# Kernel tuning notes

Hardware: AMD Instinct MI355X
Metric: run time of the kernel (lower is better)

Reference implementation:

```python
import jax, jax.numpy as jnp
import numpy as np

Z_DIM = 3
H = 128
N_BLOCKS = 4
N = 30000
E = 180000
T = 2


def _mlp2(x, W1, b1, W2, b2):
    return jnp.maximum(x @ W1 + b1, 0.0) @ W2 + b2


def _stats(x, eps=1e-8):
    # batch mean/std as accumulated by the running-stat Normalizer (buffers -> no grad)
    m = x.mean(0)
    v = jnp.maximum((x * x).mean(0) - m * m, 0.0)
    s = jnp.maximum(jnp.sqrt(v), eps)
    return jax.lax.stop_gradient(m), jax.lax.stop_gradient(s)


def setup_inputs() -> dict:
    key = jax.random.key(0)
    ks = jax.random.split(key, 32)

    def w(k, shape, fan_in):
        return jax.random.normal(k, shape, jnp.float32) / np.sqrt(fan_in).astype(np.float32)

    inp = {}
    inp["z"] = jax.random.normal(ks[0], (T, N, Z_DIM), jnp.float32)
    inp["z_target"] = jax.random.normal(ks[1], (N, Z_DIM), jnp.float32)
    inp["pos"] = jax.random.uniform(ks[2], (N, 2), jnp.float32)
    # encoder node MLP: z_dim -> H -> H
    inp["enc_node_W1"] = w(ks[3], (Z_DIM, H), Z_DIM)
    inp["enc_node_b1"] = jnp.zeros((H,), jnp.float32)
    inp["enc_node_W2"] = w(ks[4], (H, H), H)
    inp["enc_node_b2"] = jnp.zeros((H,), jnp.float32)
    # encoder edge MLP: edge_dim(3) -> H -> H
    inp["enc_edge_W1"] = w(ks[5], (3, H), 3)
    inp["enc_edge_b1"] = jnp.zeros((H,), jnp.float32)
    inp["enc_edge_W2"] = w(ks[6], (H, H), H)
    inp["enc_edge_b2"] = jnp.zeros((H,), jnp.float32)
    # decoder MLP: H -> H -> z_dim
    inp["dec_W1"] = w(ks[7], (H, H), H)
    inp["dec_b1"] = jnp.zeros((H,), jnp.float32)
    inp["dec_W2"] = w(ks[8], (H, Z_DIM), H)
    inp["dec_b2"] = jnp.zeros((Z_DIM,), jnp.float32)
    # GraphNetBlocks, stacked over n_blocks
    inp["blk_edge_W1"] = w(ks[9], (N_BLOCKS, 3 * H, H), 3 * H)
    inp["blk_edge_b1"] = jnp.zeros((N_BLOCKS, H), jnp.float32)
    inp["blk_edge_W2"] = w(ks[10], (N_BLOCKS, H, H), H)
    inp["blk_edge_b2"] = jnp.zeros((N_BLOCKS, H), jnp.float32)
    inp["blk_node_W1"] = w(ks[11], (N_BLOCKS, 2 * H, H), 2 * H)
    inp["blk_node_b1"] = jnp.zeros((N_BLOCKS, H), jnp.float32)
    inp["blk_node_W2"] = w(ks[12], (N_BLOCKS, H, H), H)
    inp["blk_node_b2"] = jnp.zeros((N_BLOCKS, H), jnp.float32)
    # bidirectional mesh edges (triangles_to_edges output)
    inp["senders"] = jax.random.randint(ks[13], (E,), 0, N, jnp.int64)
    inp["receivers"] = jax.random.randint(ks[14], (E,), 0, N, jnp.int64)
    return inp


def reference(z, z_target, pos,
              enc_node_W1, enc_node_b1, enc_node_W2, enc_node_b2,
              enc_edge_W1, enc_edge_b1, enc_edge_W2, enc_edge_b2,
              dec_W1, dec_b1, dec_W2, dec_b2,
              blk_edge_W1, blk_edge_b1, blk_edge_W2, blk_edge_b2,
              blk_node_W1, blk_node_b1, blk_node_W2, blk_node_b2,
              senders, receivers):
    zl = z[-1]                                   # [N, z_dim]
    n_nodes = zl.shape[0]

    # --- build_graph ---
    rel = pos[senders] - pos[receivers]          # [E, 2]
    ef_raw = jnp.concatenate([rel, jnp.linalg.norm(rel, axis=1, keepdims=True)], axis=1)  # [E, 3]
    em, es = _stats(ef_raw)
    ef = _mlp2((ef_raw - em) / es, enc_edge_W1, enc_edge_b1, enc_edge_W2, enc_edge_b2)    # [E, H]
    nm, ns = _stats(zl)
    nf = _mlp2((zl - nm) / ns, enc_node_W1, enc_node_b1, enc_node_W2, enc_node_b2)        # [N, H]

    # --- message passing blocks ---
    def block(carry, p):
        nf, ef = carry
        eW1, eb1, eW2, eb2, nW1, nb1, nW2, nb2 = p
        e_in = jnp.concatenate([ef, nf[senders], nf[receivers]], axis=1)   # [E, 3H]
        ef = _mlp2(e_in, eW1, eb1, eW2, eb2) + ef
        agg = jax.ops.segment_sum(ef, receivers, num_segments=n_nodes)    # [N, H]
        n_in = jnp.concatenate([nf, agg], axis=1)                          # [N, 2H]
        nf = _mlp2(n_in, nW1, nb1, nW2, nb2) + nf
        return (nf, ef), None

    (nf, ef), _ = jax.lax.scan(block, (nf, ef),
                               (blk_edge_W1, blk_edge_b1, blk_edge_W2, blk_edge_b2,
                                blk_node_W1, blk_node_b1, blk_node_W2, blk_node_b2))

    # --- decode + loss ---
    output = _mlp2(nf, dec_W1, dec_b1, dec_W2, dec_b2)                     # [N, z_dim]
    target = z_target - zl
    om, os = _stats(target)
    target_normalized = (target - om) / os
    loss = jnp.mean((target_normalized - output) ** 2)

    z_update = jax.lax.stop_gradient(output) * os + om                     # Normalizer.inverse(detach)
    z_pred = zl + z_update
    rmse = jnp.mean(jnp.sqrt(jnp.mean((z_pred - z_target) ** 2, axis=0)))
    return z_pred, loss, rmse
```

## Files before the change

### kernel.cpp

```cpp
#include <hip/hip_runtime.h>
#include <hip/hip_bf16.h>
#include <math.h>

#define HDIM 128
#define TPB 256

typedef __attribute__((ext_vector_type(8))) short bf16x8;
typedef __attribute__((ext_vector_type(4))) float f32x4;

static inline int ceil_div(int a, int b){ return (a + b - 1) / b; }

__device__ __forceinline__ float wave_sum(float v){
#pragma unroll
  for (int o = 32; o > 0; o >>= 1) v += __shfl_down(v, o, 64);
  return v;
}
__device__ __forceinline__ int wave_sum_i(int v){
#pragma unroll
  for (int o = 32; o > 0; o >>= 1) v += __shfl_down(v, o, 64);
  return v;
}

__device__ __forceinline__ short f2bf(float f){
  __hip_bfloat16 h = __float2bfloat16(f);
  return *reinterpret_cast<short*>(&h);
}
__device__ __forceinline__ float bfb2f(short s){
  unsigned int u = ((unsigned int)(unsigned short)s) << 16;
  return __builtin_bit_cast(float, u);
}

__device__ __forceinline__ void gl_lds16(const short* g, short* l){
  __builtin_amdgcn_global_load_lds(
      (const __attribute__((address_space(1))) void*)g,
      (__attribute__((address_space(3))) void*)l, 16, 0, 0);
}

__global__ void prep_a(const int* __restrict__ rcv, int* __restrict__ deg, int E, int neb,
                       const float* __restrict__ zl, const float* __restrict__ zt,
                       float* __restrict__ npart, int N, int nnb,
                       const float* __restrict__ encEW2,
                       const float* __restrict__ encNW2,
                       const float* __restrict__ decW1,
                       const float* __restrict__ beW1,
                       const float* __restrict__ beW2,
                       const float* __restrict__ bnW1,
                       const float* __restrict__ bnW2,
                       __hip_bfloat16* __restrict__ wp){
  __shared__ float red[4][12];
  const int bx = blockIdx.x, tid = threadIdx.x;
  if (bx < neb){
    int e = bx * 256 + tid;
    if (e < E) atomicAdd(&deg[rcv[e]], 1);
    return;
  }
  if (bx < neb + nnb){
    int b = bx - neb;
    int w = tid >> 6, l = tid & 63;
    int n = b * 256 + tid;
    float s[12];
#pragma unroll
    for (int i = 0; i < 12; i++) s[i] = 0.f;
    if (n < N){
#pragma unroll
      for (int d = 0; d < 3; d++){
        float z = zl[3*n+d];
        float t = zt[3*n+d] - z;
        s[d]   = z;  s[3+d] = z*z;
        s[6+d] = t;  s[9+d] = t*t;
      }
    }
#pragma unroll
    for (int i = 0; i < 12; i++) s[i] = wave_sum(s[i]);
    if (l == 0)
#pragma unroll
      for (int i = 0; i < 12; i++) red[w][i] = s[i];
    __syncthreads();
    if (tid < 12)
      npart[(size_t)b * 12 + tid] =
        red[0][tid] + red[1][tid] + red[2][tid] + red[3][tid];
    return;
  }
  int pid = bx - neb - nnb;
  int y = pid / 192;
  int x = pid - y * 192;
  const float* src; __hip_bfloat16* dst; int K;
  if (y == 0){ src = encEW2; dst = wp;          K = 128; }
  else if (y == 1){ src = encNW2; dst = wp + 16384; K = 128; }
  else if (y == 2){ src = decW1;  dst = wp + 32768; K = 128; }
  else {
    int b = (y - 3) >> 2, j = (y - 3) & 3;
    __hip_bfloat16* base = wp + 49152 + b * 114688;
    if (j == 0){ src = beW1 + b*49152; dst = base;          K = 384; }
    else if (j == 1){ src = beW2 + b*16384; dst = base + 49152; K = 128; }
    else if (j == 2){ src = bnW1 + b*32768; dst = base + 65536; K = 256; }
    else { src = bnW2 + b*16384; dst = base + 98304; K = 128; }
  }
  int id = x * 256 + tid;
  if (id >= 128 * K) return;
  int c = id >> 12;
  int r = id & 4095;
  int t = r >> 9;
  int l = (r >> 3) & 63;
  int j = r & 7;
  int k = c * 32 + ((l >> 4) << 3) + j;
  int n = t * 16 + (l & 15);
  dst[id] = __float2bfloat16(src[k * 128 + n]);
}

__global__ void scan_pass1(const int* __restrict__ deg, int* __restrict__ bsum, int N){
  __shared__ int red[4];
  int tid = threadIdx.x;
  int base = blockIdx.x * 1024;
  int s = 0;
  for (int i = tid; i < 1024; i += 256){
    int idx = base + i;
    if (idx < N) s += deg[idx];
  }
  s = wave_sum_i(s);
  if ((tid & 63) == 0) red[tid >> 6] = s;
  __syncthreads();
  if (tid == 0) bsum[blockIdx.x] = red[0] + red[1] + red[2] + red[3];
}

__global__ void scan_pass3(const int* __restrict__ deg, const int* __restrict__ bsum,
                           int nsb, int* __restrict__ cursor, int N){
  __shared__ int tsum[256];
  __shared__ int base_s;
  int tid = threadIdx.x;
  if (tid == 0){
    int acc = 0;
    for (int b = 0; b < (int)blockIdx.x; b++) acc += bsum[b];
    base_s = acc;
  }
  int base = blockIdx.x * 1024;
  int i0 = base + tid * 4;
  int v[4];
  int s = 0;
#pragma unroll
  for (int k = 0; k < 4; k++){
    int idx = i0 + k;
    v[k] = (idx < N) ? deg[idx] : 0;
    s += v[k];
  }
  tsum[tid] = s;
  __syncthreads();
  for (int off = 1; off < 256; off <<= 1){
    int val = (tid >= off) ? tsum[tid - off] : 0;
    __syncthreads();
    tsum[tid] += val;
    __syncthreads();
  }
  int excl = (tid == 0) ? 0 : tsum[tid - 1];
  int b = base_s + excl;
#pragma unroll
  for (int k = 0; k < 4; k++){
    int idx = i0 + k;
    if (idx < N){
      cursor[idx] = b;
      b += v[k];
    }
  }
}

__global__ void edge_prep(const float* __restrict__ pos,
                          const int* __restrict__ snd,
                          const int* __restrict__ rcv,
                          int* __restrict__ cursor,
                          int* __restrict__ psnd,
                          int* __restrict__ prcv,
                          float* __restrict__ ef_raw,
                          float* __restrict__ epart, int E){
  __shared__ float red[4][6];
  int tid = threadIdx.x, w = tid >> 6, l = tid & 63;
  int e = blockIdx.x * blockDim.x + tid;
  float s[6] = {0.f,0.f,0.f,0.f,0.f,0.f};
  if (e < E){
    int si = snd[e], ri = rcv[e];
    int p = atomicAdd(&cursor[ri], 1);
    psnd[p] = si;
    prcv[p] = ri;
    float rx = pos[2*si]   - pos[2*ri];
    float ry = pos[2*si+1] - pos[2*ri+1];
    float nm = sqrtf(rx*rx + ry*ry);
    ef_raw[3*p]   = rx;
    ef_raw[3*p+1] = ry;
    ef_raw[3*p+2] = nm;
    s[0] = rx; s[1] = ry; s[2] = nm;
    s[3] = rx*rx; s[4] = ry*ry; s[5] = nm*nm;
  }
#pragma unroll
  for (int k = 0; k < 6; k++) s[k] = wave_sum(s[k]);
  if (l == 0)
#pragma unroll
    for (int k = 0; k < 6; k++) red[w][k] = s[k];
  __syncthreads();
  if (tid < 6)
    epart[(size_t)blockIdx.x * 6 + tid] =
      red[0][tid] + red[1][tid] + red[2][tid] + red[3][tid];
}

__global__ void reduce_finalize(const float* __restrict__ ep, int ne,
                                const float* __restrict__ np_, int nn,
                                float* __restrict__ fin, int E, int N){
  __shared__ float red[4];
  __shared__ float raw[18];
  int tid = threadIdx.x, w = tid >> 6, l = tid & 63;
  for (int j = 0; j < 6; j++){
    float s = 0.f;
    for (int b = tid; b < ne; b += 256) s += ep[(size_t)b * 6 + j];
    s = wave_sum(s);
    if (l == 0) red[w] = s;
    __syncthreads();
    if (tid == 0) raw[j] = red[0] + red[1] + red[2] + red[3];
    __syncthreads();
  }
  for (int j = 0; j < 12; j++){
    float s = 0.f;
    for (int b = tid; b < nn; b += 256) s += np_[(size_t)b * 12 + j];
    s = wave_sum(s);
    if (l == 0) red[w] = s;
    __syncthreads();
    if (tid == 0) raw[6 + j] = red[0] + red[1] + red[2] + red[3];
    __syncthreads();
  }
  if (tid == 0){
#pragma unroll
    for (int d = 0; d < 3; d++){
      float cE = (float)E, cN = (float)N;
      float m, v;
      m = raw[0+d] / cE; v = fmaxf(raw[3+d]/cE - m*m, 0.f);
      fin[0+d] = m;  fin[3+d]  = fmaxf(sqrtf(v), 1e-8f);
      m = raw[6+d] / cN; v = fmaxf(raw[9+d]/cN - m*m, 0.f);
      fin[6+d] = m;  fin[9+d]  = fmaxf(sqrtf(v), 1e-8f);
      m = raw[12+d] / cN; v = fmaxf(raw[15+d]/cN - m*m, 0.f);
      fin[12+d] = m; fin[15+d] = fmaxf(sqrtf(v), 1e-8f);
    }
  }
}

__launch_bounds__(256)
__global__ void encoder_both(const float* __restrict__ eraw,
                             const float* __restrict__ zl,
                             const float* __restrict__ fin,
                             const float* __restrict__ eW1, const float* __restrict__ eb1,
                             const float* __restrict__ nW1, const float* __restrict__ nb1,
                             const __hip_bfloat16* __restrict__ wp,
                             const float* __restrict__ eb2, const float* __restrict__ nb2,
                             __hip_bfloat16* __restrict__ efo, __hip_bfloat16* __restrict__ nfo,
                             int E, int N, int EB){
  __shared__ __align__(16) short bsh[16384];
  const int tid = threadIdx.x, w = tid >> 6, l = tid & 63, m = l & 15, q = l >> 4;
  const bool ise = ((int)blockIdx.x < EB);
  const float* raw = ise ? eraw : zl;
  const float* mptr = fin + (ise ? 0 : 6);
  const float* sptr = fin + (ise ? 3 : 9);
  const float* W1 = ise ? eW1 : nW1;
  const float* b1 = ise ? eb1 : nb1;
  const float* b2 = ise ? eb2 : nb2;
  const short* wsrc = (const short*)wp + (ise ? 0 : 16384);
  __hip_bfloat16* out = ise ? efo : nfo;
  const int rows = ise ? E : N;
  const int bx = ise ? (int)blockIdx.x : (int)blockIdx.x - EB;
#pragma unroll
  for (int i = 0; i < 8; i++){
    int inst = w * 8 + i;
    gl_lds16(wsrc + inst * 512 + l * 8, &bsh[inst * 512]);
  }
  float s0 = mptr[0], s1 = mptr[1], s2 = mptr[2];
  float d0 = sptr[0], d1 = sptr[1], d2 = sptr[2];
  const int row0 = bx * 64 + w * 16;
  const int ra = min(row0 + m, rows - 1);
  float x0 = (raw[3*ra]   - s0) / d0;
  float x1 = (raw[3*ra+1] - s1) / d1;
  float x2 = (raw[3*ra+2] - s2) / d2;
  bf16x8 afr[4];
#pragma unroll
  for (int c = 0; c < 4; c++){
    int nb = c * 32 + q * 8;
#pragma unroll
    for (int j = 0; j < 8; j++){
      float h = b1[nb+j] + x0 * W1[nb+j] + x1 * W1[128+nb+j] + x2 * W1[256+nb+j];
      afr[c][j] = f2bf(fmaxf(h, 0.f));
    }
  }
  f32x4 acc[8];
#pragma unroll
  for (int t = 0; t < 8; t++) acc[t] = (f32x4){0.f,0.f,0.f,0.f};
  __syncthreads();
#pragma unroll
  for (int c = 0; c < 4; c++){
#pragma unroll
    for (int t = 0; t < 8; t++){
      bf16x8 b = *(const bf16x8*)&bsh[(c*8 + t)*512 + l*8];
      acc[t] = __builtin_amdgcn_mfma_f32_16x16x32_bf16(afr[c], b, acc[t], 0, 0, 0);
    }
  }
  const int row_d = row0 + q * 4;
#pragma unroll
  for (int t = 0; t < 8; t++){
    int col = t * 16 + m;
    float bb = b2[col];
#pragma unroll
    for (int r = 0; r < 4; r++){
      int e = row_d + r;
      if (e < rows) out[(size_t)e * HDIM + col] = __float2bfloat16(acc[t][r] + bb);
    }
  }
}

__launch_bounds__(256)
__global__ void msg_pre(const __hip_bfloat16* __restrict__ nf,
                        const __hip_bfloat16* __restrict__ eWf,
                        __hip_bfloat16* __restrict__ u,
                        float* __restrict__ agg, int N){
  __shared__ __align__(16) short wsh[16384];
  const int tid = threadIdx.x, w = tid >> 6, l = tid & 63, m = l & 15, q = l >> 4;
  const short* wsrc = (const short*)eWf + 4 * 4096;
#pragma unroll
  for (int i = 0; i < 8; i++){
    int f = w * 8 + i;
    gl_lds16(wsrc + f * 512 + l * 8, &wsh[f * 512]);
  }
  {
    float* az = agg + (size_t)blockIdx.x * 8192;
#pragma unroll
    for (int i = 0; i < 8; i++)
      *(f32x4*)(az + (size_t)(i * 256 + tid) * 4) = (f32x4){0.f,0.f,0.f,0.f};
  }
  const int row0 = blockIdx.x * 64 + w * 16;
  const int ra = min(row0 + m, N - 1);
  const short* pa = (const short*)nf + (size_t)ra * HDIM + q * 8;
  bf16x8 afr[4];
#pragma unroll
  for (int c = 0; c < 4; c++) afr[c] = *(const bf16x8*)(pa + c * 32);
  f32x4 acc[8];
#pragma unroll
  for (int t = 0; t < 8; t++) acc[t] = (f32x4){0.f,0.f,0.f,0.f};
  __syncthreads();
#pragma unroll
  for (int c = 0; c < 4; c++)
#pragma unroll
    for (int t = 0; t < 8; t++){
      bf16x8 b = *(const bf16x8*)&wsh[(c*8 + t)*512 + l*8];
      acc[t] = __builtin_amdgcn_mfma_f32_16x16x32_bf16(afr[c], b, acc[t], 0, 0, 0);
    }
  const int row_d = row0 + q * 4;
#pragma unroll
  for (int t = 0; t < 8; t++){
    int col = t * 16 + m;
#pragma unroll
    for (int r = 0; r < 4; r++){
      int n = row_d + r;
      if (n < N) u[(size_t)n * 256 + col] = __float2bfloat16(acc[t][r]);
    }
  }
  __syncthreads();
#pragma unroll
  for (int i = 0; i < 8; i++){
    int f = w * 8 + i;
    gl_lds16(wsrc + 16384 + f * 512 + l * 8, &wsh[f * 512]);
  }
#pragma unroll
  for (int t = 0; t < 8; t++) acc[t] = (f32x4){0.f,0.f,0.f,0.f};
  __syncthreads();
#pragma unroll
  for (int c = 0; c < 4; c++)
#pragma unroll
    for (int t = 0; t < 8; t++){
      bf16x8 b = *(const bf16x8*)&wsh[(c*8 + t)*512 + l*8];
      acc[t] = __builtin_amdgcn_mfma_f32_16x16x32_bf16(afr[c], b, acc[t], 0, 0, 0);
    }
#pragma unroll
  for (int t = 0; t < 8; t++){
    int col = 128 + t * 16 + m;
#pragma unroll
    for (int r = 0; r < 4; r++){
      int n = row_d + r;
      if (n < N) u[(size_t)n * 256 + col] = __float2bfloat16(acc[t][r]);
    }
  }
}

__launch_bounds__(512)
__global__ void edge_block(const int* __restrict__ psnd,
                           const int* __restrict__ prcv,
                           const __hip_bfloat16* __restrict__ u,
                           __hip_bfloat16* __restrict__ ef,
                           const __hip_bfloat16* __restrict__ Wfrag,
                           const float* __restrict__ b1,
                           const float* __restrict__ b2,
                           float* __restrict__ agg,
                           int do_write, int E){
  __shared__ __align__(16) short bsh[16384];
  __shared__ __align__(16) short hsh[8][16][136];
  __shared__ int rsh[128];
  const int tid = threadIdx.x, w = tid >> 6, l = tid & 63, m = l & 15, q = l >> 4;
  const short* wsrc = (const short*)Wfrag;
  const int row0 = blockIdx.x * 128 + w * 16;
  const int grow = min(row0 + (l >> 2), E - 1);
  const int us_row = psnd[grow], ur_row = prcv[grow];
  if ((l & 3) == 0) rsh[w * 16 + (l >> 2)] = ur_row;
#pragma unroll
  for (int i = 0; i < 4; i++){
    int inst = i * 8 + w;
    gl_lds16(wsrc + inst * 512 + l * 8, &bsh[inst * 512]);
  }
  const int ra = min(row0 + m, E - 1);
  const short* pe = (const short*)ef + (size_t)ra * HDIM + q * 8;
  bf16x8 afr[4];
#pragma unroll
  for (int c = 0; c < 4; c++) afr[c] = *(const bf16x8*)(pe + c * 32);
  {
    const short* pus = (const short*)u + (size_t)us_row * 256 + (l & 3) * 32;
    const short* pur = (const short*)u + (size_t)ur_row * 256 + 128 + (l & 3) * 32;
    short* hdst = &hsh[w][l >> 2][(l & 3) * 32];
#pragma unroll
    for (int k = 0; k < 4; k++){
      bf16x8 a = *(const bf16x8*)(pus + k * 8);
      bf16x8 b = *(const bf16x8*)(pur + k * 8);
      bf16x8 s;
#pragma unroll
      for (int j = 0; j < 8; j++) s[j] = f2bf(bfb2f(a[j]) + bfb2f(b[j]));
      *(bf16x8*)(hdst + k * 8) = s;
    }
  }
  f32x4 acc[8];
#pragma unroll
  for (int t = 0; t < 8; t++) acc[t] = (f32x4){0.f,0.f,0.f,0.f};
  __syncthreads();
#pragma unroll
  for (int c = 0; c < 4; c++){
#pragma unroll
    for (int t = 0; t < 8; t++){
      bf16x8 b = *(const bf16x8*)&bsh[(c*8 + t)*512 + l*8];
      acc[t] = __builtin_amdgcn_mfma_f32_16x16x32_bf16(afr[c], b, acc[t], 0, 0, 0);
    }
  }
  __syncthreads();
#pragma unroll
  for (int i = 0; i < 4; i++){
    int inst = i * 8 + w;
    gl_lds16(wsrc + 49152 + inst * 512 + l * 8, &bsh[inst * 512]);
  }
#pragma unroll
  for (int t = 0; t < 8; t++){
    float bb = b1[t * 16 + m];
#pragma unroll
    for (int r = 0; r < 4; r++){
      float uval = bfb2f(hsh[w][q*4 + r][t*16 + m]);
      hsh[w][q*4 + r][t*16 + m] = f2bf(fmaxf(acc[t][r] + uval + bb, 0.f));
    }
  }
  __syncthreads();
  bf16x8 ah[4];
  const short* ph = &hsh[w][m][0] + q * 8;
#pragma unroll
  for (int c = 0; c < 4; c++) ah[c] = *(const bf16x8*)(ph + c * 32);
#pragma unroll
  for (int t = 0; t < 8; t++) acc[t] = (f32x4){0.f,0.f,0.f,0.f};
#pragma unroll
  for (int c = 0; c < 4; c++){
#pragma unroll
    for (int t = 0; t < 8; t++){
      bf16x8 b = *(const bf16x8*)&bsh[(c*8 + t)*512 + l*8];
      acc[t] = __builtin_amdgcn_mfma_f32_16x16x32_bf16(ah[c], b, acc[t], 0, 0, 0);
    }
  }
#pragma unroll
  for (int t = 0; t < 8; t++){
    float bb = b2[t * 16 + m];
#pragma unroll
    for (int r = 0; r < 4; r++)
      hsh[w][q*4 + r][t*16 + m] = f2bf(acc[t][r] + bb);
  }
  const int orow = row0 + (l >> 2);
  const int orc = min(orow, E - 1);
  const short* pold = (const short*)ef + (size_t)orc * HDIM + (l & 3) * 32;
  short* hslot = &hsh[w][l >> 2][(l & 3) * 32];
  short* dst = (short*)ef + (size_t)orc * HDIM + (l & 3) * 32;
  const bool wr = (orow < E) && do_write;
#pragma unroll
  for (int k = 0; k < 4; k++){
    bf16x8 vnew = *(const bf16x8*)(hslot + k * 8);
    bf16x8 vo   = *(const bf16x8*)(pold + k * 8);
    bf16x8 vr;
#pragma unroll
    for (int j = 0; j < 8; j++) vr[j] = f2bf(bfb2f(vnew[j]) + bfb2f(vo[j]));
    *(bf16x8*)(hslot + k * 8) = vr;
    if (wr) *(bf16x8*)(dst + k * 8) = vr;
  }
  __syncthreads();
  {
    const int c = tid & 127;
    const int g = tid >> 7;
    const int nval = min(128, E - (int)blockIdx.x * 128);
    const int e0 = g * 32;
    if (e0 < nval){
      const int e1 = min(e0 + 32, nval);
      float run = 0.f; int cur = -1; int runstart = e0;
#pragma unroll
      for (int half = 0; half < 2; half++){
        float v[16]; int rv[16];
#pragma unroll
        for (int k = 0; k < 16; k++){
          int e = e0 + half * 16 + k;
          v[k]  = bfb2f(hsh[(e >> 4) & 7][e & 15][c]);
          rv[k] = rsh[e & 127];
        }
#pragma unroll
        for (int k = 0; k < 16; k++){
          int e = e0 + half * 16 + k;
          if (e < e1){
            if (rv[k] != cur){
              if (cur >= 0){
                if (runstart == e0) atomicAdd(&agg[(size_t)cur * 128 + c], run);
                else                agg[(size_t)cur * 128 + c] = run;
              }
              cur = rv[k]; run = 0.f; runstart = e;
            }
            run += v[k];
          }
        }
      }
      atomicAdd(&agg[(size_t)cur * 128 + c], run);
    }
  }
}

#define NB_COMPUTE_CHUNK(c) do {                                               \
  const short* bb_ = &bsh[(((c) >> 1) & 1) * 8192 + ((c) & 1) * 4096];         \
  _Pragma("unroll")                                                            \
  for (int t = 0; t < 8; t++){                                                 \
    bf16x8 b = *(const bf16x8*)(bb_ + t * 512 + l * 8);                        \
    acc[t] = __builtin_amdgcn_mfma_f32_16x16x32_bf16(afr[c], b, acc[t], 0, 0, 0); \
  }                                                                            \
} while(0)

__launch_bounds__(256)
__global__ void node_block(const float* __restrict__ agg,
                           __hip_bfloat16* __restrict__ nf,
                           const __hip_bfloat16* __restrict__ Wfrag,
                           const float* __restrict__ b1,
                           const float* __restrict__ b2,
                           int N){
  __shared__ __align__(16) short bsh[16384];
  __shared__ __align__(16) short hsh[4][16][136];
  const int tid = threadIdx.x, w = tid >> 6, l = tid & 63, m = l & 15, q = l >> 4;
  const short* wsrc = (const short*)Wfrag;
  auto stage_pair = [&](int p){
    const short* s = wsrc + p * 8192;
    short* d = &bsh[(p & 1) * 8192];
#pragma unroll
    for (int i = 0; i < 4; i++)
      gl_lds16(s + (i*4 + w)*512 + l*8, d + (i*4 + w)*512);
  };
  stage_pair(0); stage_pair(1);

  const int row0 = blockIdx.x * 64 + w * 16;
  const int ra = min(row0 + m, N - 1);
  const short* pn = (const short*)nf + (size_t)ra * HDIM + q * 8;
  bf16x8 afr[8];
#pragma unroll
  for (int c = 0; c < 4; c++) afr[c] = *(const bf16x8*)(pn + c * 32);

  const float* pag = agg + (size_t)ra * 128 + q * 8;
#pragma unroll
  for (int c = 0; c < 4; c++){
    f32x4 a0 = *(const f32x4*)(pag + c * 32);
    f32x4 a1 = *(const f32x4*)(pag + c * 32 + 4);
#pragma unroll
    for (int j = 0; j < 4; j++){
      afr[4 + c][j]     = f2bf(a0[j]);
      afr[4 + c][4 + j] = f2bf(a1[j]);
    }
  }

  f32x4 acc[8];
#pragma unroll
  for (int t = 0; t < 8; t++) acc[t] = (f32x4){0.f,0.f,0.f,0.f};
  __syncthreads();
  NB_COMPUTE_CHUNK(0);
  NB_COMPUTE_CHUNK(1);
  __syncthreads();
  stage_pair(2);
  NB_COMPUTE_CHUNK(2);
  NB_COMPUTE_CHUNK(3);
  __syncthreads();
  stage_pair(3);
  NB_COMPUTE_CHUNK(4);
  NB_COMPUTE_CHUNK(5);
  __syncthreads();
  NB_COMPUTE_CHUNK(6);
  NB_COMPUTE_CHUNK(7);
  __syncthreads();
  {
    const short* s = wsrc + 32768;
#pragma unroll
    for (int i = 0; i < 8; i++)
      gl_lds16(s + (i*4 + w)*512 + l*8, &bsh[(i*4 + w)*512]);
  }
#pragma unroll
  for (int t = 0; t < 8; t++){
    float bb = b1[t * 16 + m];
#pragma unroll
    for (int r = 0; r < 4; r++)
      hsh[w][q*4 + r][t*16 + m] = f2bf(fmaxf(acc[t][r] + bb, 0.f));
  }
  __syncthreads();
  const short* ph = &hsh[w][m][0] + q * 8;
#pragma unroll
  for (int t = 0; t < 8; t++) acc[t] = (f32x4){0.f,0.f,0.f,0.f};
#pragma unroll
  for (int c = 0; c < 4; c++){
    bf16x8 a = *(const bf16x8*)(ph + c * 32);
#pragma unroll
    for (int t = 0; t < 8; t++){
      bf16x8 b = *(const bf16x8*)&bsh[(c*8 + t)*512 + l*8];
      acc[t] = __builtin_amdgcn_mfma_f32_16x16x32_bf16(a, b, acc[t], 0, 0, 0);
    }
  }
#pragma unroll
  for (int t = 0; t < 8; t++){
    float bb = b2[t * 16 + m];
#pragma unroll
    for (int r = 0; r < 4; r++)
      hsh[w][q*4 + r][t*16 + m] = f2bf(acc[t][r] + bb);
  }
  const int orow = row0 + (l >> 2);
  if (orow < N){
    const short* pold = (const short*)nf + (size_t)orow * HDIM + (l & 3) * 32;
    const short* src = &hsh[w][l >> 2][(l & 3) * 32];
    short* dst = (short*)nf + (size_t)orow * HDIM + (l & 3) * 32;
#pragma unroll
    for (int k = 0; k < 4; k++){
      bf16x8 vnew = *(const bf16x8*)(src + k * 8);
      bf16x8 vo   = *(const bf16x8*)(pold + k * 8);
      bf16x8 vr;
#pragma unroll
      for (int j = 0; j < 8; j++) vr[j] = f2bf(bfb2f(vnew[j]) + bfb2f(vo[j]));
      *(bf16x8*)(dst + k * 8) = vr;
    }
  }
}

__launch_bounds__(256)
__global__ void dec_fused(const __hip_bfloat16* __restrict__ A,
                          const __hip_bfloat16* __restrict__ Wf,
                          const float* __restrict__ b1,
                          const float* __restrict__ W2,
                          const float* __restrict__ b2,
                          const float* __restrict__ zl,
                          const float* __restrict__ z_target,
                          const float* __restrict__ fin,
                          float* __restrict__ d_out,
                          float* __restrict__ lred,
                          unsigned int* __restrict__ cnt,
                          int N){
  __shared__ __align__(16) short bsh[16384];
  __shared__ float Wl[HDIM * 3];
  __shared__ float red[4][4];
  const int tid = threadIdx.x, w = tid >> 6, l = tid & 63, m = l & 15, q = l >> 4;
  const short* wsrc = (const short*)Wf;
#pragma unroll
  for (int i = 0; i < 8; i++){
    int inst = w * 8 + i;
    gl_lds16(wsrc + inst * 512 + l * 8, &bsh[inst * 512]);
  }
  for (int i = tid; i < HDIM * 3; i += 256) Wl[i] = W2[i];
  const int row0 = blockIdx.x * 64 + w * 16;
  const int ra = min(row0 + m, N - 1);
  const short* pa = (const short*)A + (size_t)ra * HDIM + q * 8;
  bf16x8 afr[4];
#pragma unroll
  for (int c = 0; c < 4; c++) afr[c] = *(const bf16x8*)(pa + c * 32);
  f32x4 acc[8];
#pragma unroll
  for (int t = 0; t < 8; t++) acc[t] = (f32x4){0.f,0.f,0.f,0.f};
  __syncthreads();
#pragma unroll
  for (int c = 0; c < 4; c++){
#pragma unroll
    for (int t = 0; t < 8; t++){
      bf16x8 b = *(const bf16x8*)&bsh[(c*8 + t)*512 + l*8];
      acc[t] = __builtin_amdgcn_mfma_f32_16x16x32_bf16(afr[c], b, acc[t], 0, 0, 0);
    }
  }
  float p0[4] = {0,0,0,0}, p1[4] = {0,0,0,0}, p2[4] = {0,0,0,0};
#pragma unroll
  for (int t = 0; t < 8; t++){
    int col = t * 16 + m;
    float bb = b1[col];
    float w0 = Wl[col*3], w1 = Wl[col*3+1], w2 = Wl[col*3+2];
#pragma unroll
    for (int r = 0; r < 4; r++){
      float h = fmaxf(acc[t][r] + bb, 0.f);
      p0[r] += h * w0; p1[r] += h * w1; p2[r] += h * w2;
    }
  }
#pragma unroll
  for (int r = 0; r < 4; r++){
#pragma unroll
    for (int o = 1; o < 16; o <<= 1){
      p0[r] += __shfl_xor(p0[r], o, 64);
      p1[r] += __shfl_xor(p1[r], o, 64);
      p2[r] += __shfl_xor(p2[r], o, 64);
    }
  }
  float s[4] = {0.f,0.f,0.f,0.f};
  if (m == 0){
#pragma unroll
    for (int r = 0; r < 4; r++){
      int n = row0 + q * 4 + r;
      if (n < N){
        float pd[3] = {p0[r], p1[r], p2[r]};
#pragma unroll
        for (int d = 0; d < 3; d++){
          float o   = pd[d] + b2[d];
          float om = fin[12 + d], os = fin[15 + d];
          float zld = zl[3*n + d];
          float zt  = z_target[3*n + d];
          float tn  = ((zt - zld) - om) / os;
          float diff = tn - o;
          s[0] += diff * diff;
          float zp = zld + o * os + om;
          d_out[3*n + d] = zp;
          float e = zp - zt;
          s[1 + d] += e * e;
        }
      }
    }
  }
#pragma unroll
  for (int k = 0; k < 4; k++) s[k] = wave_sum(s[k]);
  if (l == 0)
#pragma unroll
    for (int k = 0; k < 4; k++) red[w][k] = s[k];
  __syncthreads();
  if (tid < 4)
    atomicAdd(&lred[tid], red[0][tid] + red[1][tid] + red[2][tid] + red[3][tid]);
  __syncthreads();
  if (tid == 0){
    __threadfence();
    unsigned int t = atomicAdd(cnt, 1u);
    if (t == gridDim.x - 1){
      float vals[4];
#pragma unroll
      for (int k = 0; k < 4; k++) vals[k] = atomicAdd(&lred[k], 0.f);
      float cN = (float)N;
      float loss = vals[0] / (3.f * cN);
      float rmse = (sqrtf(vals[1]/cN) + sqrtf(vals[2]/cN) + sqrtf(vals[3]/cN)) / 3.f;
      d_out[(size_t)3 * N]     = loss;
      d_out[(size_t)3 * N + 1] = rmse;
    }
  }
}

extern "C" void kernel_launch(void* const* d_in, const int* in_sizes, int n_in,
                              void* d_out, int out_size, void* d_ws, size_t ws_size,
                              hipStream_t stream){
  const float* z           = (const float*)d_in[0];
  const float* z_target    = (const float*)d_in[1];
  const float* pos         = (const float*)d_in[2];
  const float* enc_node_W1 = (const float*)d_in[3];
  const float* enc_node_b1 = (const float*)d_in[4];
  const float* enc_node_W2 = (const float*)d_in[5];
  const float* enc_node_b2 = (const float*)d_in[6];
  const float* enc_edge_W1 = (const float*)d_in[7];
  const float* enc_edge_b1 = (const float*)d_in[8];
  const float* enc_edge_W2 = (const float*)d_in[9];
  const float* enc_edge_b2 = (const float*)d_in[10];
  const float* dec_W1      = (const float*)d_in[11];
  const float* dec_b1      = (const float*)d_in[12];
  const float* dec_W2      = (const float*)d_in[13];
  const float* dec_b2      = (const float*)d_in[14];
  const float* blk_edge_W1 = (const float*)d_in[15];
  const float* blk_edge_b1 = (const float*)d_in[16];
  const float* blk_edge_W2 = (const float*)d_in[17];
  const float* blk_edge_b2 = (const float*)d_in[18];
  const float* blk_node_W1 = (const float*)d_in[19];
  const float* blk_node_b1 = (const float*)d_in[20];
  const float* blk_node_W2 = (const float*)d_in[21];
  const float* blk_node_b2 = (const float*)d_in[22];
  const int*   senders     = (const int*)d_in[23];
  const int*   receivers   = (const int*)d_in[24];

  const int N = in_sizes[1] / 3;
  const int E = in_sizes[23];
  const float* zl = z + (size_t)N * 3;

  const int neb = ceil_div(E, TPB);
  const int nnb = ceil_div(N, TPB);
  const int nsb = ceil_div(N, 1024);
  const int EB  = ceil_div(E, 64);
  const int NB  = ceil_div(N, 64);

  char* p = (char*)d_ws;
  auto carve = [&](size_t bytes) -> char* {
    char* r = p; p += (bytes + 255) & ~(size_t)255; return r;
  };
  float* stats_fin = (float*)carve(32 * 4);
  float* epart     = (float*)carve((size_t)neb * 6 * 4);
  float* npart     = (float*)carve((size_t)nnb * 12 * 4);
  float* ef_raw    = (float*)carve((size_t)E * 3 * 4);
  int*   deg       = (int*)carve((size_t)(N + 16) * 4);
  float* lred      = (float*)(deg + N);
  unsigned int* cnt = (unsigned int*)(deg + N + 4);
  int*   bsum      = (int*)carve((size_t)(nsb + 1) * 4);
  int*   cursor    = (int*)carve((size_t)N * 4);
  int*   psnd      = (int*)carve((size_t)E * 4);
  int*   prcv      = (int*)carve((size_t)E * 4);
  float* agg       = (float*)carve(((size_t)N + 64) * 128 * 4);
  __hip_bfloat16* wp = (__hip_bfloat16*)carve((size_t)507904 * 2);
  __hip_bfloat16* ef = (__hip_bfloat16*)carve((size_t)E * HDIM * 2);
  __hip_bfloat16* nf = (__hip_bfloat16*)carve((size_t)N * HDIM * 2);
  __hip_bfloat16* u  = (__hip_bfloat16*)carve((size_t)N * 256 * 2);

  float* out = (float*)d_out;

  hipMemsetAsync(deg, 0, (size_t)(N + 16) * 4, stream);

  prep_a<<<neb + nnb + 3648, TPB, 0, stream>>>(receivers, deg, E, neb,
                                               zl, z_target, npart, N, nnb,
                                               enc_edge_W2, enc_node_W2, dec_W1,
                                               blk_edge_W1, blk_edge_W2,
                                               blk_node_W1, blk_node_W2, wp);
  scan_pass1<<<nsb, TPB, 0, stream>>>(deg, bsum, N);
  scan_pass3<<<nsb, TPB, 0, stream>>>(deg, bsum, nsb, cursor, N);
  edge_prep<<<neb, TPB, 0, stream>>>(pos, senders, receivers, cursor,
                                     psnd, prcv, ef_raw, epart, E);
  reduce_finalize<<<1, TPB, 0, stream>>>(epart, neb, npart, nnb, stats_fin, E, N);

  encoder_both<<<EB + NB, TPB, 0, stream>>>(ef_raw, zl, stats_fin,
                                            enc_edge_W1, enc_edge_b1,
                                            enc_node_W1, enc_node_b1,
                                            wp, enc_edge_b2, enc_node_b2,
                                            ef, nf, E, N, EB);

  for (int b = 0; b < 4; b++){
    const __hip_bfloat16* eWf = wp + 49152 + (size_t)b * 114688;
    const __hip_bfloat16* nWf = eWf + 65536;
    const float* eb1 = blk_edge_b1 + (size_t)b * 128;
    const float* eb2 = blk_edge_b2 + (size_t)b * 128;
    const float* nb1 = blk_node_b1 + (size_t)b * 128;
    const float* nb2 = blk_node_b2 + (size_t)b * 128;

    msg_pre<<<NB, TPB, 0, stream>>>(nf, eWf, u, agg, N);
    edge_block<<<ceil_div(E, 128), 512, 0, stream>>>(psnd, prcv, u, ef,
                                                     eWf, eb1, eb2, agg,
                                                     (b < 3) ? 1 : 0, E);
    node_block<<<NB, TPB, 0, stream>>>(agg, nf, nWf, nb1, nb2, N);
  }

  dec_fused<<<NB, TPB, 0, stream>>>(nf, wp + 32768, dec_b1, dec_W2, dec_b2,
                                    zl, z_target, stats_fin,
                                    out, lred, cnt, N);
}
```

Before: 488.9 us.

## Fuse stats finalize, next-block msg_pre, and decoder into producer kernels

Folds the single-block reduce_finalize into edge_prep as a last-block-done reduction using an atomic counter. Fuses the next block's msg_pre (node projection into u and zeroing agg) into the tail of node_block, and the decoder into the final node_block via a mode flag. The aim is fewer kernel launches and one fewer reload of node features per block. The cost is more LDS and registers in node_block, plus a serial last-block tail in edge_prep.

```diff
diff --git a/kernel.cpp b/kernel.cpp
--- a/kernel.cpp
+++ b/kernel.cpp
@@ -170,8 +170,15 @@
                           int* __restrict__ psnd,
                           int* __restrict__ prcv,
                           float* __restrict__ ef_raw,
-                          float* __restrict__ epart, int E){
+                          float* __restrict__ epart,
+                          const float* __restrict__ npart, int nn,
+                          float* __restrict__ fin,
+                          unsigned int* __restrict__ ep_cnt,
+                          int E, int N){
   __shared__ float red[4][6];
+  __shared__ float rawS[18];
+  __shared__ float redS[4];
+  __shared__ int doneS;
   int tid = threadIdx.x, w = tid >> 6, l = tid & 63;
   int e = blockIdx.x * blockDim.x + tid;
   float s[6] = {0.f,0.f,0.f,0.f,0.f,0.f};
@@ -198,30 +205,31 @@
   if (tid < 6)
     epart[(size_t)blockIdx.x * 6 + tid] =
       red[0][tid] + red[1][tid] + red[2][tid] + red[3][tid];
-}
-
-__global__ void reduce_finalize(const float* __restrict__ ep, int ne,
-                                const float* __restrict__ np_, int nn,
-                                float* __restrict__ fin, int E, int N){
-  __shared__ float red[4];
-  __shared__ float raw[18];
-  int tid = threadIdx.x, w = tid >> 6, l = tid & 63;
+  __syncthreads();
+  if (tid == 0){
+    __threadfence();
+    unsigned int t = atomicAdd(ep_cnt, 1u);
+    doneS = (t == gridDim.x - 1);
+  }
+  __syncthreads();
+  if (!doneS) return;
+  const int ne = gridDim.x;
   for (int j = 0; j < 6; j++){
-    float s = 0.f;
-    for (int b = tid; b < ne; b += 256) s += ep[(size_t)b * 6 + j];
-    s = wave_sum(s);
-    if (l == 0) red[w] = s;
-    __syncthreads();
-    if (tid == 0) raw[j] = red[0] + red[1] + red[2] + red[3];
+    float t = 0.f;
+    for (int b = tid; b < ne; b += 256) t += epart[(size_t)b * 6 + j];
+    t = wave_sum(t);
+    if (l == 0) redS[w] = t;
+    __syncthreads();
+    if (tid == 0) rawS[j] = redS[0] + redS[1] + redS[2] + redS[3];
     __syncthreads();
   }
   for (int j = 0; j < 12; j++){
-    float s = 0.f;
-    for (int b = tid; b < nn; b += 256) s += np_[(size_t)b * 12 + j];
-    s = wave_sum(s);
-    if (l == 0) red[w] = s;
-    __syncthreads();
-    if (tid == 0) raw[6 + j] = red[0] + red[1] + red[2] + red[3];
+    float t = 0.f;
+    for (int b = tid; b < nn; b += 256) t += npart[(size_t)b * 12 + j];
+    t = wave_sum(t);
+    if (l == 0) redS[w] = t;
+    __syncthreads();
+    if (tid == 0) rawS[6 + j] = redS[0] + redS[1] + redS[2] + redS[3];
     __syncthreads();
   }
   if (tid == 0){
@@ -229,11 +237,11 @@
     for (int d = 0; d < 3; d++){
       float cE = (float)E, cN = (float)N;
       float m, v;
-      m = raw[0+d] / cE; v = fmaxf(raw[3+d]/cE - m*m, 0.f);
+      m = rawS[0+d] / cE; v = fmaxf(rawS[3+d]/cE - m*m, 0.f);
       fin[0+d] = m;  fin[3+d]  = fmaxf(sqrtf(v), 1e-8f);
-      m = raw[6+d] / cN; v = fmaxf(raw[9+d]/cN - m*m, 0.f);
+      m = rawS[6+d] / cN; v = fmaxf(rawS[9+d]/cN - m*m, 0.f);
       fin[6+d] = m;  fin[9+d]  = fmaxf(sqrtf(v), 1e-8f);
-      m = raw[12+d] / cN; v = fmaxf(raw[15+d]/cN - m*m, 0.f);
+      m = rawS[12+d] / cN; v = fmaxf(rawS[15+d]/cN - m*m, 0.f);
       fin[12+d] = m; fin[15+d] = fmaxf(sqrtf(v), 1e-8f);
     }
   }
@@ -543,9 +551,25 @@
                            const __hip_bfloat16* __restrict__ Wfrag,
                            const float* __restrict__ b1,
                            const float* __restrict__ b2,
+                           const __hip_bfloat16* __restrict__ eWf_next,
+                           __hip_bfloat16* __restrict__ u,
+                           float* __restrict__ aggz,
+                           int mode,
+                           const __hip_bfloat16* __restrict__ decWf,
+                           const float* __restrict__ db1,
+                           const float* __restrict__ dW2,
+                           const float* __restrict__ db2,
+                           const float* __restrict__ zl,
+                           const float* __restrict__ z_target,
+                           const float* __restrict__ fin,
+                           float* __restrict__ d_out,
+                           float* __restrict__ lred,
+                           unsigned int* __restrict__ cnt,
                            int N){
   __shared__ __align__(16) short bsh[16384];
   __shared__ __align__(16) short hsh[4][16][136];
+  __shared__ float Wl[HDIM * 3];
+  __shared__ float redS[4][4];
   const int tid = threadIdx.x, w = tid >> 6, l = tid & 63, m = l & 15, q = l >> 4;
   const short* wsrc = (const short*)Wfrag;
   auto stage_pair = [&](int p){
@@ -580,6 +604,12 @@
 #pragma unroll
   for (int t = 0; t < 8; t++) acc[t] = (f32x4){0.f,0.f,0.f,0.f};
   __syncthreads();
+  if (mode == 0){
+    float* az = aggz + (size_t)blockIdx.x * 8192;
+#pragma unroll
+    for (int i = 0; i < 8; i++)
+      *(f32x4*)(az + (size_t)(i * 256 + tid) * 4) = (f32x4){0.f,0.f,0.f,0.f};
+  }
   NB_COMPUTE_CHUNK(0);
   NB_COMPUTE_CHUNK(1);
   __syncthreads();
@@ -627,131 +657,170 @@
     for (int r = 0; r < 4; r++)
       hsh[w][q*4 + r][t*16 + m] = f2bf(acc[t][r] + bb);
   }
-  const int orow = row0 + (l >> 2);
-  if (orow < N){
-    const short* pold = (const short*)nf + (size_t)orow * HDIM + (l & 3) * 32;
-    const short* src = &hsh[w][l >> 2][(l & 3) * 32];
-    short* dst = (short*)nf + (size_t)orow * HDIM + (l & 3) * 32;
+  {
+    const int orow = row0 + (l >> 2);
+    const int orc = min(orow, N - 1);
+    const short* pold = (const short*)nf + (size_t)orc * HDIM + (l & 3) * 32;
+    short* hslot = &hsh[w][l >> 2][(l & 3) * 32];
+    short* dst = (short*)nf + (size_t)orc * HDIM + (l & 3) * 32;
+    const bool wr = (orow < N) && (mode == 0);
 #pragma unroll
     for (int k = 0; k < 4; k++){
-      bf16x8 vnew = *(const bf16x8*)(src + k * 8);
+      bf16x8 vnew = *(const bf16x8*)(hslot + k * 8);
       bf16x8 vo   = *(const bf16x8*)(pold + k * 8);
       bf16x8 vr;
 #pragma unroll
       for (int j = 0; j < 8; j++) vr[j] = f2bf(bfb2f(vnew[j]) + bfb2f(vo[j]));
-      *(bf16x8*)(dst + k * 8) = vr;
-    }
-  }
-}
-
-__launch_bounds__(256)
-__global__ void dec_fused(const __hip_bfloat16* __restrict__ A,
-                          const __hip_bfloat16* __restrict__ Wf,
-                          const float* __restrict__ b1,
-                          const float* __restrict__ W2,
-                          const float* __restrict__ b2,
-                          const float* __restrict__ zl,
-                          const float* __restrict__ z_target,
-                          const float* __restrict__ fin,
-                          float* __restrict__ d_out,
-                          float* __restrict__ lred,
-                          unsigned int* __restrict__ cnt,
-                          int N){
-  __shared__ __align__(16) short bsh[16384];
-  __shared__ float Wl[HDIM * 3];
-  __shared__ float red[4][4];
-  const int tid = threadIdx.x, w = tid >> 6, l = tid & 63, m = l & 15, q = l >> 4;
-  const short* wsrc = (const short*)Wf;
-#pragma unroll
-  for (int i = 0; i < 8; i++){
-    int inst = w * 8 + i;
-    gl_lds16(wsrc + inst * 512 + l * 8, &bsh[inst * 512]);
-  }
-  for (int i = tid; i < HDIM * 3; i += 256) Wl[i] = W2[i];
-  const int row0 = blockIdx.x * 64 + w * 16;
-  const int ra = min(row0 + m, N - 1);
-  const short* pa = (const short*)A + (size_t)ra * HDIM + q * 8;
-  bf16x8 afr[4];
-#pragma unroll
-  for (int c = 0; c < 4; c++) afr[c] = *(const bf16x8*)(pa + c * 32);
-  f32x4 acc[8];
-#pragma unroll
-  for (int t = 0; t < 8; t++) acc[t] = (f32x4){0.f,0.f,0.f,0.f};
-  __syncthreads();
-#pragma unroll
-  for (int c = 0; c < 4; c++){
+      *(bf16x8*)(hslot + k * 8) = vr;
+      if (wr) *(bf16x8*)(dst + k * 8) = vr;
+    }
+  }
+
+  if (mode == 0){
+    const short* ws = (const short*)eWf_next + 4 * 4096;
+#pragma unroll
+    for (int i = 0; i < 8; i++){
+      int f = w * 8 + i;
+      gl_lds16(ws + f * 512 + l * 8, &bsh[f * 512]);
+    }
+    __syncthreads();
+    bf16x8 a2[4];
+    const short* ph2 = &hsh[w][m][0] + q * 8;
+#pragma unroll
+    for (int c = 0; c < 4; c++) a2[c] = *(const bf16x8*)(ph2 + c * 32);
+#pragma unroll
+    for (int t = 0; t < 8; t++) acc[t] = (f32x4){0.f,0.f,0.f,0.f};
+#pragma unroll
+    for (int c = 0; c < 4; c++)
+#pragma unroll
+      for (int t = 0; t < 8; t++){
+        bf16x8 b = *(const bf16x8*)&bsh[(c*8 + t)*512 + l*8];
+        acc[t] = __builtin_amdgcn_mfma_f32_16x16x32_bf16(a2[c], b, acc[t], 0, 0, 0);
+      }
+    const int row_d = row0 + q * 4;
 #pragma unroll
     for (int t = 0; t < 8; t++){
-      bf16x8 b = *(const bf16x8*)&bsh[(c*8 + t)*512 + l*8];
-      acc[t] = __builtin_amdgcn_mfma_f32_16x16x32_bf16(afr[c], b, acc[t], 0, 0, 0);
-    }
-  }
-  float p0[4] = {0,0,0,0}, p1[4] = {0,0,0,0}, p2[4] = {0,0,0,0};
-#pragma unroll
-  for (int t = 0; t < 8; t++){
-    int col = t * 16 + m;
-    float bb = b1[col];
-    float w0 = Wl[col*3], w1 = Wl[col*3+1], w2 = Wl[col*3+2];
+      int col = t * 16 + m;
+#pragma unroll
+      for (int r = 0; r < 4; r++){
+        int n = row_d + r;
+        if (n < N) u[(size_t)n * 256 + col] = __float2bfloat16(acc[t][r]);
+      }
+    }
+    __syncthreads();
+#pragma unroll
+    for (int i = 0; i < 8; i++){
+      int f = w * 8 + i;
+      gl_lds16(ws + 16384 + f * 512 + l * 8, &bsh[f * 512]);
+    }
+#pragma unroll
+    for (int t = 0; t < 8; t++) acc[t] = (f32x4){0.f,0.f,0.f,0.f};
+    __syncthreads();
+#pragma unroll
+    for (int c = 0; c < 4; c++)
+#pragma unroll
+      for (int t = 0; t < 8; t++){
+        bf16x8 b = *(const bf16x8*)&bsh[(c*8 + t)*512 + l*8];
+        acc[t] = __builtin_amdgcn_mfma_f32_16x16x32_bf16(a2[c], b, acc[t], 0, 0, 0);
+      }
+#pragma unroll
+    for (int t = 0; t < 8; t++){
+      int col = 128 + t * 16 + m;
+#pragma unroll
+      for (int r = 0; r < 4; r++){
+        int n = row_d + r;
+        if (n < N) u[(size_t)n * 256 + col] = __float2bfloat16(acc[t][r]);
+      }
+    }
+  } else {
+    const short* ws = (const short*)decWf;
+#pragma unroll
+    for (int i = 0; i < 8; i++){
+      int f = w * 8 + i;
+      gl_lds16(ws + f * 512 + l * 8, &bsh[f * 512]);
+    }
+    for (int i = tid; i < HDIM * 3; i += 256) Wl[i] = dW2[i];
+    __syncthreads();
+    bf16x8 a2[4];
+    const short* ph2 = &hsh[w][m][0] + q * 8;
+#pragma unroll
+    for (int c = 0; c < 4; c++) a2[c] = *(const bf16x8*)(ph2 + c * 32);
+#pragma unroll
+    for (int t = 0; t < 8; t++) acc[t] = (f32x4){0.f,0.f,0.f,0.f};
+#pragma unroll
+    for (int c = 0; c < 4; c++)
+#pragma unroll
+      for (int t = 0; t < 8; t++){
+        bf16x8 b = *(const bf16x8*)&bsh[(c*8 + t)*512 + l*8];
+        acc[t] = __builtin_amdgcn_mfma_f32_16x16x32_bf16(a2[c], b, acc[t], 0, 0, 0);
+      }
+    float p0[4] = {0,0,0,0}, p1[4] = {0,0,0,0}, p2[4] = {0,0,0,0};
+#pragma unroll
+    for (int t = 0; t < 8; t++){
+      int col = t * 16 + m;
+      float bb = db1[col];
+      float w0 = Wl[col*3], w1 = Wl[col*3+1], w2 = Wl[col*3+2];
+#pragma unroll
+      for (int r = 0; r < 4; r++){
+        float h = fmaxf(acc[t][r] + bb, 0.f);
+        p0[r] += h * w0; p1[r] += h * w1; p2[r] += h * w2;
+      }
+    }
 #pragma unroll
     for (int r = 0; r < 4; r++){
-      float h = fmaxf(acc[t][r] + bb, 0.f);
-      p0[r] += h * w0; p1[r] += h * w1; p2[r] += h * w2;
-    }
-  }
-#pragma unroll
-  for (int r = 0; r < 4; r++){
-#pragma unroll
-    for (int o = 1; o < 16; o <<= 1){
-      p0[r] += __shfl_xor(p0[r], o, 64);
-      p1[r] += __shfl_xor(p1[r], o, 64);
-      p2[r] += __shfl_xor(p2[r], o, 64);
-    }
-  }
-  float s[4] = {0.f,0.f,0.f,0.f};
-  if (m == 0){
-#pragma unroll
-    for (int r = 0; r < 4; r++){
-      int n = row0 + q * 4 + r;
-      if (n < N){
-        float pd[3] = {p0[r], p1[r], p2[r]};
-#pragma unroll
-        for (int d = 0; d < 3; d++){
-          float o   = pd[d] + b2[d];
-          float om = fin[12 + d], os = fin[15 + d];
-          float zld = zl[3*n + d];
-          float zt  = z_target[3*n + d];
-          float tn  = ((zt - zld) - om) / os;
-          float diff = tn - o;
-          s[0] += diff * diff;
-          float zp = zld + o * os + om;
-          d_out[3*n + d] = zp;
-          float e = zp - zt;
-          s[1 + d] += e * e;
+#pragma unroll
+      for (int o = 1; o < 16; o <<= 1){
+        p0[r] += __shfl_xor(p0[r], o, 64);
+        p1[r] += __shfl_xor(p1[r], o, 64);
+        p2[r] += __shfl_xor(p2[r], o, 64);
+      }
+    }
+    float s[4] = {0.f,0.f,0.f,0.f};
+    if (m == 0){
+#pragma unroll
+      for (int r = 0; r < 4; r++){
+        int n = row0 + q * 4 + r;
+        if (n < N){
+          float pd[3] = {p0[r], p1[r], p2[r]};
+#pragma unroll
+          for (int d = 0; d < 3; d++){
+            float o   = pd[d] + db2[d];
+            float om = fin[12 + d], os = fin[15 + d];
+            float zld = zl[3*n + d];
+            float zt  = z_target[3*n + d];
+            float tn  = ((zt - zld) - om) / os;
+            float diff = tn - o;
+            s[0] += diff * diff;
+            float zp = zld + o * os + om;
+            d_out[3*n + d] = zp;
+            float e = zp - zt;
+            s[1 + d] += e * e;
+          }
         }
       }
     }
-  }
-#pragma unroll
-  for (int k = 0; k < 4; k++) s[k] = wave_sum(s[k]);
-  if (l == 0)
-#pragma unroll
-    for (int k = 0; k < 4; k++) red[w][k] = s[k];
-  __syncthreads();
-  if (tid < 4)
-    atomicAdd(&lred[tid], red[0][tid] + red[1][tid] + red[2][tid] + red[3][tid]);
-  __syncthreads();
-  if (tid == 0){
-    __threadfence();
-    unsigned int t = atomicAdd(cnt, 1u);
-    if (t == gridDim.x - 1){
-      float vals[4];
-#pragma unroll
-      for (int k = 0; k < 4; k++) vals[k] = atomicAdd(&lred[k], 0.f);
-      float cN = (float)N;
-      float loss = vals[0] / (3.f * cN);
-      float rmse = (sqrtf(vals[1]/cN) + sqrtf(vals[2]/cN) + sqrtf(vals[3]/cN)) / 3.f;
-      d_out[(size_t)3 * N]     = loss;
-      d_out[(size_t)3 * N + 1] = rmse;
+#pragma unroll
+    for (int k = 0; k < 4; k++) s[k] = wave_sum(s[k]);
+    if (l == 0)
+#pragma unroll
+      for (int k = 0; k < 4; k++) redS[w][k] = s[k];
+    __syncthreads();
+    if (tid < 4)
+      atomicAdd(&lred[tid], redS[0][tid] + redS[1][tid] + redS[2][tid] + redS[3][tid]);
+    __syncthreads();
+    if (tid == 0){
+      __threadfence();
+      unsigned int t = atomicAdd(cnt, 1u);
+      if (t == gridDim.x - 1){
+        float vals[4];
+#pragma unroll
+        for (int k = 0; k < 4; k++) vals[k] = atomicAdd(&lred[k], 0.f);
+        float cN = (float)N;
+        float loss = vals[0] / (3.f * cN);
+        float rmse = (sqrtf(vals[1]/cN) + sqrtf(vals[2]/cN) + sqrtf(vals[3]/cN)) / 3.f;
+        d_out[(size_t)3 * N]     = loss;
+        d_out[(size_t)3 * N + 1] = rmse;
+      }
     }
   }
 }
@@ -805,7 +874,8 @@
   float* ef_raw    = (float*)carve((size_t)E * 3 * 4);
   int*   deg       = (int*)carve((size_t)(N + 16) * 4);
   float* lred      = (float*)(deg + N);
-  unsigned int* cnt = (unsigned int*)(deg + N + 4);
+  unsigned int* cnt    = (unsigned int*)(deg + N + 4);
+  unsigned int* ep_cnt = (unsigned int*)(deg + N + 5);
   int*   bsum      = (int*)carve((size_t)(nsb + 1) * 4);
   int*   cursor    = (int*)carve((size_t)N * 4);
   int*   psnd      = (int*)carve((size_t)E * 4);
@@ -828,14 +898,16 @@
   scan_pass1<<<nsb, TPB, 0, stream>>>(deg, bsum, N);
   scan_pass3<<<nsb, TPB, 0, stream>>>(deg, bsum, nsb, cursor, N);
   edge_prep<<<neb, TPB, 0, stream>>>(pos, senders, receivers, cursor,
-                                     psnd, prcv, ef_raw, epart, E);
-  reduce_finalize<<<1, TPB, 0, stream>>>(epart, neb, npart, nnb, stats_fin, E, N);
+                                     psnd, prcv, ef_raw, epart,
+                                     npart, nnb, stats_fin, ep_cnt, E, N);
 
   encoder_both<<<EB + NB, TPB, 0, stream>>>(ef_raw, zl, stats_fin,
                                             enc_edge_W1, enc_edge_b1,
                                             enc_node_W1, enc_node_b1,
                                             wp, enc_edge_b2, enc_node_b2,
                                             ef, nf, E, N, EB);
+
+  msg_pre<<<NB, TPB, 0, stream>>>(nf, wp + 49152, u, agg, N);
 
   for (int b = 0; b < 4; b++){
     const __hip_bfloat16* eWf = wp + 49152 + (size_t)b * 114688;
@@ -844,15 +916,17 @@
     const float* eb2 = blk_edge_b2 + (size_t)b * 128;
     const float* nb1 = blk_node_b1 + (size_t)b * 128;
     const float* nb2 = blk_node_b2 + (size_t)b * 128;
-
-    msg_pre<<<NB, TPB, 0, stream>>>(nf, eWf, u, agg, N);
+    const __hip_bfloat16* eWf_next =
+        wp + 49152 + (size_t)((b + 1) & 3) * 114688;
+
     edge_block<<<ceil_div(E, 128), 512, 0, stream>>>(psnd, prcv, u, ef,
                                                      eWf, eb1, eb2, agg,
                                                      (b < 3) ? 1 : 0, E);
-    node_block<<<NB, TPB, 0, stream>>>(agg, nf, nWf, nb1, nb2, N);
-  }
-
-  dec_fused<<<NB, TPB, 0, stream>>>(nf, wp + 32768, dec_b1, dec_W2, dec_b2,
-                                    zl, z_target, stats_fin,
-                                    out, lred, cnt, N);
-}
+    node_block<<<NB, TPB, 0, stream>>>(agg, nf, nWf, nb1, nb2,
+                                       eWf_next, u, agg,
+                                       (b < 3) ? 0 : 1,
+                                       wp + 32768, dec_b1, dec_W2, dec_b2,
+                                       zl, z_target, stats_fin,
+                                       out, lred, cnt, N);
+  }
+}
```

Measured after the change: 500.9 us. 1.02x slower.
